# Kernel tuning notes

Hardware: AMD Instinct MI355X
Metric: run time of the kernel (lower is better)

Reference implementation:

```python
import jax, jax.numpy as jnp
import numpy as np

H = 128  # hidden_dim
COORD_CLAMP = 100.0


def _glorot(key, shape):
    fan_in, fan_out = shape[0], shape[1]
    lim = float(np.sqrt(6.0 / (fan_in + fan_out)))
    return jax.random.uniform(key, shape, jnp.float32, -lim, lim)


def setup_inputs() -> dict:
    key = jax.random.key(0)
    ks = jax.random.split(key, 20)
    B, N = 2, 512
    inp = {
        "h": jax.random.normal(ks[0], (B, N, H), jnp.float32),
        "pos": jax.random.normal(ks[1], (B, N, 3), jnp.float32),
        "vel": jax.random.normal(ks[2], (B, N, 3), jnp.float32),
        # edge_mlp: Linear(2H+2 -> H), SiLU, Linear(H -> H), SiLU
        "We1": _glorot(ks[3], (2 * H + 2, H)), "be1": jnp.zeros((H,), jnp.float32),
        "We2": _glorot(ks[4], (H, H)), "be2": jnp.zeros((H,), jnp.float32),
        # attention_mlp: Linear(H -> 1), Sigmoid
        "Wa": _glorot(ks[5], (H, 1)), "ba": jnp.zeros((1,), jnp.float32),
        # pos_mlp: Linear(H -> H), SiLU, Linear(H -> 1, no bias)
        "Wp1": _glorot(ks[6], (H, H)), "bp1": jnp.zeros((H,), jnp.float32),
        "Wp2": _glorot(ks[7], (H, 1)),
        # vel_mlp: Linear(H -> H), SiLU, Linear(H -> 1, no bias)
        "Wv1": _glorot(ks[8], (H, H)), "bv1": jnp.zeros((H,), jnp.float32),
        "Wv2": _glorot(ks[9], (H, 1)),
        # node_mlp: Linear(2H -> H), SiLU, Linear(H -> H)
        "Wn1": _glorot(ks[10], (2 * H, H)), "bn1": jnp.zeros((H,), jnp.float32),
        "Wn2": _glorot(ks[11], (H, H)), "bn2": jnp.zeros((H,), jnp.float32),
    }
    return inp


def reference(h, pos, vel, We1, be1, We2, be2, Wa, ba,
              Wp1, bp1, Wp2, Wv1, bv1, Wv2, Wn1, bn1, Wn2, bn2):
    B, N, _ = pos.shape
    # pairwise diffs: [B, N, N, 3]
    pos_diff = pos[:, :, None, :] - pos[:, None, :, :]
    vel_diff = vel[:, :, None, :] - vel[:, None, :, :]
    pos_dist_sq = jnp.sum(pos_diff ** 2, axis=-1, keepdims=True)  # [B,N,N,1]
    vel_dist_sq = jnp.sum(vel_diff ** 2, axis=-1, keepdims=True)
    h_i = jnp.broadcast_to(h[:, :, None, :], (B, N, N, H))
    h_j = jnp.broadcast_to(h[:, None, :, :], (B, N, N, H))
    edge_input = jnp.concatenate([h_i, h_j, pos_dist_sq, vel_dist_sq], axis=-1)  # [B,N,N,2H+2]
    # edge MLP
    m = jax.nn.silu(jnp.einsum('bijc,ch->bijh', edge_input, We1) + be1)
    m_ij = jax.nn.silu(jnp.einsum('bijh,hk->bijk', m, We2) + be2)
    # attention gate
    att = jax.nn.sigmoid(jnp.einsum('bijh,ho->bijo', m_ij, Wa) + ba)  # [B,N,N,1]
    m_ij = m_ij * att
    # tanh-weighted coordinate/velocity updates
    pos_w = jnp.tanh(jnp.einsum('bijh,ho->bijo', jax.nn.silu(jnp.einsum('bijh,hk->bijk', m_ij, Wp1) + bp1), Wp2))
    vel_w = jnp.tanh(jnp.einsum('bijh,ho->bijo', jax.nn.silu(jnp.einsum('bijh,hk->bijk', m_ij, Wv1) + bv1), Wv2))
    denom = jnp.float32(max(N - 1, 1))
    pos_update = jnp.sum(pos_diff * pos_w, axis=2) / denom  # [B,N,3]
    vel_update = jnp.sum(vel_diff * vel_w, axis=2) / denom
    pos_out = jnp.clip(pos + pos_update, -COORD_CLAMP, COORD_CLAMP)
    vel_out = jnp.clip(vel + vel_update, -COORD_CLAMP, COORD_CLAMP)
    # node update
    m_agg = jnp.sum(m_ij, axis=2)  # [B,N,H]
    node_input = jnp.concatenate([h, m_agg], axis=-1)  # [B,N,2H]
    h_out = jax.nn.silu(jnp.einsum('bnc,ch->bnh', node_input, Wn1) + bn1)
    h_out = jnp.einsum('bnh,hk->bnk', h_out, Wn2) + bn2
    h_out = h + h_out  # residual
    return (h_out, pos_out, vel_out)
```

## Files before the change

kernel.cpp:

```cpp
#include <hip/hip_runtime.h>
#include <hip/hip_bf16.h>

#define Hd 128
#define Nn 512
#define TJ 32
#define LSTRIDE 136

typedef __bf16 bf16x8 __attribute__((ext_vector_type(8)));
typedef float  floatx4 __attribute__((ext_vector_type(4)));

__device__ __forceinline__ float frcp(float x){ return __builtin_amdgcn_rcpf(x); }
__device__ __forceinline__ float fsilu(float x){ return x * frcp(1.f + __expf(-x)); }
__device__ __forceinline__ float fsigm(float x){ return frcp(1.f + __expf(-x)); }
__device__ __forceinline__ float ftanh(float x){ return 1.f - 2.f * frcp(__expf(2.f*x) + 1.f); }
__device__ __forceinline__ float rfl(float x){
  return __int_as_float(__builtin_amdgcn_readfirstlane(__float_as_int(x)));
}

__global__ __launch_bounds__(256) void prep(const float* __restrict__ h,
                                            const float* __restrict__ We1,
                                            const float* __restrict__ be1,
                                            const float* __restrict__ We2,
                                            const float* __restrict__ Wp1,
                                            const float* __restrict__ Wv1,
                                            float* __restrict__ A,
                                            float* __restrict__ Bm,
                                            __bf16* __restrict__ dst,
                                            float* __restrict__ zbase){
  if (blockIdx.x < 1024){
    const int row = blockIdx.x;
    const int k = threadIdx.x & 127, ch = threadIdx.x >> 7;
    __shared__ float hL[Hd];
    __shared__ float pa[2][Hd], pb[2][Hd];
    if (threadIdx.x < Hd) hL[threadIdx.x] = h[row*Hd + threadIdx.x];
    __syncthreads();
    float a0=0.f,a1=0.f, b0=0.f,b1=0.f;
    const int cbase = ch*64;
    #pragma unroll 8
    for (int cc = 0; cc < 64; cc += 2){
      const int c = cbase + cc;
      a0 += hL[c]   * We1[c*Hd + k];
      a1 += hL[c+1] * We1[(c+1)*Hd + k];
      b0 += hL[c]   * We1[(c+Hd)*Hd + k];
      b1 += hL[c+1] * We1[(c+1+Hd)*Hd + k];
    }
    pa[ch][k] = a0 + a1;
    pb[ch][k] = b0 + b1;
    __syncthreads();
    if (threadIdx.x < Hd){
      A[row*Hd + k]  = pa[0][k] + pa[1][k] + be1[k];
      Bm[row*Hd + k] = pb[0][k] + pb[1][k];
    }
  } else if (blockIdx.x < 1048){
    const int blk = blockIdx.x - 1024;
    const int which = blk >> 3, m = blk & 7;
    const float* src = (which == 0) ? We2 : (which == 1 ? Wp1 : Wv1);
    __bf16* d = dst + which * (Hd*Hd);
    #pragma unroll
    for (int it = 0; it < 8; ++it){
      const int sidx = m*2048 + it*256 + threadIdx.x;
      const int kk = sidx >> 7, cc = sidx & 127;
      const int s = kk >> 5, j = kk & 7;
      const int lane = ((kk >> 3) & 3)*16 + (cc & 15);
      const int n = cc >> 4;
      d[n*2048 + s*512 + lane*8 + j] = (__bf16)src[sidx];
    }
  } else {
    const int t0 = (blockIdx.x - 1048)*256 + threadIdx.x;
    for (int idx = t0; idx < 137216; idx += 2048) zbase[idx] = 0.f;
  }
}

__device__ __forceinline__ void gemm_kloop(const __bf16* __restrict__ buf,
                                           const bf16x8* __restrict__ Bs,
                                           int w, int lane, int q, int l15,
                                           floatx4 acc[2][2]){
  const floatx4 zero = {0.f, 0.f, 0.f, 0.f};
  #pragma unroll
  for (int m = 0; m < 2; ++m){ acc[m][0] = zero; acc[m][1] = zero; }
  #pragma unroll
  for (int s = 0; s < 4; ++s){
    bf16x8 af[2];
    #pragma unroll
    for (int m = 0; m < 2; ++m)
      af[m] = *(const bf16x8*)&buf[(16*m + l15)*LSTRIDE + s*32 + q*8];
    const bf16x8 b0 = Bs[((2*w + 0)*4 + s)*64 + lane];
    const bf16x8 b1 = Bs[((2*w + 1)*4 + s)*64 + lane];
    #pragma unroll
    for (int m = 0; m < 2; ++m){
      acc[m][0] = __builtin_amdgcn_mfma_f32_16x16x32_bf16(af[m], b0, acc[m][0], 0, 0, 0);
      acc[m][1] = __builtin_amdgcn_mfma_f32_16x16x32_bf16(af[m], b1, acc[m][1], 0, 0, 0);
    }
  }
}

__device__ __forceinline__ float fold_reduce8(float pr[8], int lane){
  #pragma unroll
  for (int k = 0; k < 4; ++k){
    const float send = (lane & 1) ? pr[k] : pr[k+4];
    const float recv = __shfl_xor(send, 1, 64);
    pr[k] = ((lane & 1) ? pr[k+4] : pr[k]) + recv;
  }
  #pragma unroll
  for (int k = 0; k < 2; ++k){
    const float send = (lane & 2) ? pr[k] : pr[k+2];
    const float recv = __shfl_xor(send, 2, 64);
    pr[k] = ((lane & 2) ? pr[k+2] : pr[k]) + recv;
  }
  {
    const float send = (lane & 4) ? pr[0] : pr[1];
    const float recv = __shfl_xor(send, 4, 64);
    pr[0] = ((lane & 4) ? pr[1] : pr[0]) + recv;
  }
  pr[0] += __shfl_xor(pr[0], 8, 64);
  return pr[0];
}
__device__ __forceinline__ int bitrev3(int x){
  return ((x&1)<<2) | (x&2) | ((x&4)>>2);
}

__device__ __forceinline__ void wdot_epilogue(floatx4 acc[2][2],
                                              const float att[2][4],
                                              const float* __restrict__ biasL,
                                              const float* __restrict__ wG,
                                              int w, int lane, int q, int l15,
                                              float (*part)[TJ]){
  float pr[8];
  #pragma unroll
  for (int k = 0; k < 8; ++k) pr[k] = 0.f;
  const int c0 = 32*w + l15, c1 = c0 + 16;
  const float bb0 = biasL[c0], bb1 = biasL[c1];
  const float ww0 = wG[c0],    ww1 = wG[c1];
  #pragma unroll
  for (int m = 0; m < 2; ++m){
    #pragma unroll
    for (int r = 0; r < 4; ++r){
      pr[4*m + r] += fsilu(fmaf(att[m][r], acc[m][0][r], bb0)) * ww0;
      pr[4*m + r] += fsilu(fmaf(att[m][r], acc[m][1][r], bb1)) * ww1;
    }
  }
  const float v = fold_reduce8(pr, lane);
  if ((lane & 15) < 8){
    const int k = bitrev3(l15 & 7);
    part[w][16*(k >> 2) + 4*q + (k & 3)] = v;
  }
}

__global__ __launch_bounds__(256) void egnn_main(
    const float* __restrict__ pos, const float* __restrict__ vel,
    const float* __restrict__ We1, const float* __restrict__ be2,
    const float* __restrict__ Wa,  const float* __restrict__ ba,
    const float* __restrict__ bp1, const float* __restrict__ Wp2,
    const float* __restrict__ bv1, const float* __restrict__ Wv2,
    const float* __restrict__ A,   const float* __restrict__ Bm,
    const __bf16* __restrict__ Wsw,
    float* __restrict__ magg, float* __restrict__ posu, float* __restrict__ velu){

  const int t    = threadIdx.x;
  const int w    = t >> 6;
  const int lane = t & 63;
  const int q    = lane >> 4;
  const int l15  = lane & 15;
  const int node = blockIdx.x >> 1;
  const int half = blockIdx.x & 1;
  const int b    = node >> 9;
  const int i    = node & (Nn - 1);

  __shared__ float AiL[Hd], wpL[Hd], wvL[Hd], be2L[Hd], bp1L[Hd], bv1L[Hd];
  __shared__ __align__(16) __bf16 bufm [TJ*LSTRIDE];
  __shared__ __align__(16) __bf16 bufij[TJ*LSTRIDE];
  __shared__ float partAtt[4][TJ], partP[4][TJ], partV[4][TJ];
  __shared__ float attL[TJ];

  if (t < Hd){
    AiL[t]  = A[node*Hd + t];
    wpL[t]  = We1[256*Hd + t];
    wvL[t]  = We1[257*Hd + t];
    be2L[t] = be2[t]; bp1L[t] = bp1[t]; bv1L[t] = bv1[t];
  }
  const float baV = ba[0];
  const float* pi = &pos[(size_t)node*3];
  const float* vi = &vel[(size_t)node*3];
  const float px = rfl(pi[0]), py = rfl(pi[1]), pz = rfl(pi[2]);
  const float ux = rfl(vi[0]), uy = rfl(vi[1]), uz = rfl(vi[2]);
  __syncthreads();

  const bf16x8* We2s = (const bf16x8*)(Wsw);
  const bf16x8* Wp1s = (const bf16x8*)(Wsw + Hd*Hd);
  const bf16x8* Wv1s = (const bf16x8*)(Wsw + 2*Hd*Hd);

  float accR[8];
  #pragma unroll
  for (int e = 0; e < 8; ++e) accR[e] = 0.f;

  for (int jt = 0; jt < (Nn/2)/TJ; ++jt){
    const int j0 = half*(Nn/2) + jt * TJ;

    {
      const int j = t >> 3, seg = t & 7;
      const int jg = j0 + j;
      const float* pj = &pos[(size_t)(b*Nn + jg)*3];
      const float* vj = &vel[(size_t)(b*Nn + jg)*3];
      const float dx = px - pj[0], dy = py - pj[1], dz = pz - pj[2];
      const float dp = dx*dx + dy*dy + dz*dz;
      const float ex = ux - vj[0], ey = uy - vj[1], ez = uz - vj[2];
      const float dv = ex*ex + ey*ey + ez*ez;
      const floatx4* A4  = (const floatx4*)&AiL[seg*16];
      const floatx4* wp4 = (const floatx4*)&wpL[seg*16];
      const floatx4* wv4 = (const floatx4*)&wvL[seg*16];
      const floatx4* Bp4 = (const floatx4*)&Bm[((size_t)(b*Nn + jg))*Hd + seg*16];
      bf16x8* dstp = (bf16x8*)&bufm[j*LSTRIDE + seg*16];
      #pragma unroll
      for (int u = 0; u < 2; ++u){
        union { bf16x8 v; __hip_bfloat162 h2[4]; } o;
        #pragma unroll
        for (int v2 = 0; v2 < 2; ++v2){
          const floatx4 av = A4[u*2+v2], wpv = wp4[u*2+v2];
          const floatx4 wvv = wv4[u*2+v2], bv = Bp4[u*2+v2];
          float x[4];
          #pragma unroll
          for (int e = 0; e < 4; ++e)
            x[e] = fsilu(av[e] + bv[e] + dp*wpv[e] + dv*wvv[e]);
          o.h2[v2*2+0] = __float22bfloat162_rn(make_float2(x[0], x[1]));
          o.h2[v2*2+1] = __float22bfloat162_rn(make_float2(x[2], x[3]));
        }
        dstp[u] = o.v;
      }
    }
    __syncthreads();

    {
      floatx4 acc[2][2];
      gemm_kloop(bufm, We2s, w, lane, q, l15, acc);
      float aw[8];
      #pragma unroll
      for (int k = 0; k < 8; ++k) aw[k] = 0.f;
      const int c0 = 32*w + l15, c1 = c0 + 16;
      const float bb0 = be2L[c0], bb1 = be2L[c1];
      const float wa0 = Wa[c0],   wa1 = Wa[c1];
      #pragma unroll
      for (int m = 0; m < 2; ++m){
        #pragma unroll
        for (int r = 0; r < 4; ++r){
          const int row = 16*m + 4*q + r;
          const float sv0 = fsilu(acc[m][0][r] + bb0);
          const float sv1 = fsilu(acc[m][1][r] + bb1);
          bufij[row*LSTRIDE + c0] = (__bf16)sv0;
          bufij[row*LSTRIDE + c1] = (__bf16)sv1;
          aw[4*m + r] += sv0*wa0 + sv1*wa1;
        }
      }
      const float v = fold_reduce8(aw, lane);
      if (l15 < 8){
        const int k = bitrev3(l15);
        partAtt[w][16*(k >> 2) + 4*q + (k & 3)] = v;
      }
    }
    __syncthreads();

    {
      const int rowX = (16*(l15 & 3) + 4*q + (l15 >> 2)) & (TJ - 1);
      const float attv = fsigm(partAtt[0][rowX] + partAtt[1][rowX] +
                               partAtt[2][rowX] + partAtt[3][rowX] + baV);
      if (w == 3 && (l15 & 3) < 2) attL[rowX] = attv;
      floatx4 acc[2][2];
      gemm_kloop(bufij, Wp1s, w, lane, q, l15, acc);
      float att[2][4];
      #pragma unroll
      for (int m = 0; m < 2; ++m)
        #pragma unroll
        for (int r = 0; r < 4; ++r)
          att[m][r] = __shfl(attv, 16*q + 4*r + m, 64);
      wdot_epilogue(acc, att, bp1L, Wp2, w, lane, q, l15, partP);
      gemm_kloop(bufij, Wv1s, w, lane, q, l15, acc);
      wdot_epilogue(acc, att, bv1L, Wv2, w, lane, q, l15, partV);
    }
    __syncthreads();

    if (w == 0){
      if (lane < TJ){
        const int jg = j0 + lane;
        const float* pj = &pos[(size_t)(b*Nn + jg)*3];
        const float s4 = partP[0][lane] + partP[1][lane] + partP[2][lane] + partP[3][lane];
        const float pw = ftanh(s4);
        accR[0] += (px - pj[0]) * pw;
        accR[1] += (py - pj[1]) * pw;
        accR[2] += (pz - pj[2]) * pw;
      }
    } else if (w == 1){
      if (lane < TJ){
        const int jg = j0 + lane;
        const float* vj = &vel[(size_t)(b*Nn + jg)*3];
        const float s4 = partV[0][lane] + partV[1][lane] + partV[2][lane] + partV[3][lane];
        const float vw = ftanh(s4);
        accR[0] += (ux - vj[0]) * vw;
        accR[1] += (uy - vj[1]) * vw;
        accR[2] += (uz - vj[2]) * vw;
      }
    } else {
      const int sg   = (w - 2)*8 + (lane & 7);
      const int jsub = lane >> 3;
      #pragma unroll
      for (int jj = 0; jj < 4; ++jj){
        const int j = jj*8 + jsub;
        const float aj = attL[j];
        const bf16x8 v = *(const bf16x8*)&bufij[j*LSTRIDE + sg*8];
        #pragma unroll
        for (int e = 0; e < 8; ++e) accR[e] += aj * (float)v[e];
      }
    }
  }

  if (w == 0 || w == 1){
    float v0 = accR[0], v1 = accR[1], v2 = accR[2];
    #pragma unroll
    for (int off = 1; off < 64; off <<= 1){
      v0 += __shfl_xor(v0, off, 64);
      v1 += __shfl_xor(v1, off, 64);
      v2 += __shfl_xor(v2, off, 64);
    }
    if (lane == 0){
      float* dst = (w == 0) ? &posu[node*3] : &velu[node*3];
      atomicAdd(&dst[0], v0);
      atomicAdd(&dst[1], v1);
      atomicAdd(&dst[2], v2);
    }
  } else {
    const int sg = (w - 2)*8 + (lane & 7);
    #pragma unroll
    for (int off = 8; off < 64; off <<= 1){
      #pragma unroll
      for (int e = 0; e < 8; ++e) accR[e] += __shfl_xor(accR[e], off, 64);
    }
    if ((lane >> 3) == 0){
      #pragma unroll
      for (int e = 0; e < 8; ++e)
        atomicAdd(&magg[node*Hd + sg*8 + e], accR[e]);
    }
  }
}

__global__ __launch_bounds__(256) void egnn_final(
    const float* __restrict__ h, const float* __restrict__ pos, const float* __restrict__ vel,
    const float* __restrict__ Wn1, const float* __restrict__ bn1,
    const float* __restrict__ Wn2, const float* __restrict__ bn2,
    const float* __restrict__ magg, const float* __restrict__ posu,
    const float* __restrict__ velu, float* __restrict__ out){
  const int row = blockIdx.x;
  const int t = threadIdx.x;
  const int k = t & 127, ch = t >> 7;
  __shared__ float ni[2*Hd];
  __shared__ float p1[2][Hd], t1[Hd];
  ni[t] = (t < Hd) ? h[row*Hd + t] : magg[row*Hd + (t - Hd)];
  __syncthreads();
  {
    float a0=0.f,a1=0.f,a2=0.f,a3=0.f;
    const int cb = ch*Hd;
    #pragma unroll 8
    for (int cc = 0; cc < Hd; cc += 4){
      a0 += ni[cb+cc+0] * Wn1[(cb+cc+0)*Hd + k];
      a1 += ni[cb+cc+1] * Wn1[(cb+cc+1)*Hd + k];
      a2 += ni[cb+cc+2] * Wn1[(cb+cc+2)*Hd + k];
      a3 += ni[cb+cc+3] * Wn1[(cb+cc+3)*Hd + k];
    }
    p1[ch][k] = (a0+a1)+(a2+a3);
  }
  __syncthreads();
  if (t < Hd) t1[t] = fsilu(p1[0][t] + p1[1][t] + bn1[t]);
  __syncthreads();
  {
    float a0=0.f,a1=0.f,a2=0.f,a3=0.f;
    const int cb = ch*64;
    #pragma unroll 8
    for (int cc = 0; cc < 64; cc += 4){
      a0 += t1[cb+cc+0] * Wn2[(cb+cc+0)*Hd + k];
      a1 += t1[cb+cc+1] * Wn2[(cb+cc+1)*Hd + k];
      a2 += t1[cb+cc+2] * Wn2[(cb+cc+2)*Hd + k];
      a3 += t1[cb+cc+3] * Wn2[(cb+cc+3)*Hd + k];
    }
    p1[ch][k] = (a0+a1)+(a2+a3);
  }
  __syncthreads();
  if (t < Hd){
    out[row*Hd + t] = ni[t] + p1[0][t] + p1[1][t] + bn2[t];
  } else if (t < Hd + 3){
    const int d = t - Hd;
    const float v = pos[row*3 + d] + posu[row*3 + d] * (1.f/511.f);
    out[2*Nn*Hd + row*3 + d] = fminf(fmaxf(v, -100.f), 100.f);
  } else if (t < Hd + 6){
    const int d = t - Hd - 3;
    const float v = vel[row*3 + d] + velu[row*3 + d] * (1.f/511.f);
    out[2*Nn*Hd + 2*Nn*3 + row*3 + d] = fminf(fmaxf(v, -100.f), 100.f);
  }
}

extern "C" void kernel_launch(void* const* d_in, const int* in_sizes, int n_in,
                              void* d_out, int out_size, void* d_ws, size_t ws_size,
                              hipStream_t stream){
  const float* h   = (const float*)d_in[0];
  const float* pos = (const float*)d_in[1];
  const float* vel = (const float*)d_in[2];
  const float* We1 = (const float*)d_in[3];
  const float* be1 = (const float*)d_in[4];
  const float* We2 = (const float*)d_in[5];
  const float* be2 = (const float*)d_in[6];
  const float* Wa  = (const float*)d_in[7];
  const float* ba  = (const float*)d_in[8];
  const float* Wp1 = (const float*)d_in[9];
  const float* bp1 = (const float*)d_in[10];
  const float* Wp2 = (const float*)d_in[11];
  const float* Wv1 = (const float*)d_in[12];
  const float* bv1 = (const float*)d_in[13];
  const float* Wv2 = (const float*)d_in[14];
  const float* Wn1 = (const float*)d_in[15];
  const float* bn1 = (const float*)d_in[16];
  const float* Wn2 = (const float*)d_in[17];
  const float* bn2 = (const float*)d_in[18];

  float* ws = (float*)d_ws;
  float*  A    = ws;
  float*  Bmm  = ws + 131072;
  float*  magg = ws + 262144;
  float*  posu = ws + 393216;
  float*  velu = ws + 396288;
  __bf16* Wsw  = (__bf16*)(ws + 399360);

  prep      <<<dim3(1056), dim3(256), 0, stream>>>(h, We1, be1, We2, Wp1, Wv1,
                                                   A, Bmm, Wsw, magg);
  egnn_main <<<dim3(2048), dim3(256), 0, stream>>>(pos, vel, We1, be2, Wa, ba, bp1, Wp2,
                                                   bv1, Wv2, A, Bmm, Wsw, magg, posu, velu);
  egnn_final<<<dim3(1024), dim3(256), 0, stream>>>(h, pos, vel, Wn1, bn1, Wn2, bn2,
                                                   magg, posu, velu, (float*)d_out);
}
```

Before: 248.3 us.

## Fuse node MLP into main kernel via last-block counter and batch prep rows

Drops the separate egnn_final launch. The last of the two half-blocks per node, found with an atomic counter and a threadfence, now runs the node MLP and the position/velocity clamp inside egnn_main. The prep kernel now handles 4 rows per block so each We1 load is reused across rows, which cuts the grid from 1056 to 288 blocks. This saves a kernel launch and a global round trip, at the cost of extra atomics and fences in every main block. The zeroing range is extended so the counters are cleared each call.

```diff
diff --git a/kernel.cpp b/kernel.cpp
--- a/kernel.cpp
+++ b/kernel.cpp
@@ -27,32 +27,40 @@
                                             float* __restrict__ Bm,
                                             __bf16* __restrict__ dst,
                                             float* __restrict__ zbase){
-  if (blockIdx.x < 1024){
-    const int row = blockIdx.x;
+  if (blockIdx.x < 256){
+    const int r0 = blockIdx.x * 4;
     const int k = threadIdx.x & 127, ch = threadIdx.x >> 7;
-    __shared__ float hL[Hd];
-    __shared__ float pa[2][Hd], pb[2][Hd];
-    if (threadIdx.x < Hd) hL[threadIdx.x] = h[row*Hd + threadIdx.x];
+    __shared__ float hL[4][Hd];
+    __shared__ float pa[2][4][Hd], pb[2][4][Hd];
+    for (int idx = threadIdx.x; idx < 4*Hd; idx += 256)
+      hL[idx >> 7][idx & 127] = h[r0*Hd + idx];
     __syncthreads();
-    float a0=0.f,a1=0.f, b0=0.f,b1=0.f;
+    float a[4] = {0.f,0.f,0.f,0.f}, bb[4] = {0.f,0.f,0.f,0.f};
     const int cbase = ch*64;
-    #pragma unroll 8
-    for (int cc = 0; cc < 64; cc += 2){
+    #pragma unroll 4
+    for (int cc = 0; cc < 64; ++cc){
       const int c = cbase + cc;
-      a0 += hL[c]   * We1[c*Hd + k];
-      a1 += hL[c+1] * We1[(c+1)*Hd + k];
-      b0 += hL[c]   * We1[(c+Hd)*Hd + k];
-      b1 += hL[c+1] * We1[(c+1+Hd)*Hd + k];
-    }
-    pa[ch][k] = a0 + a1;
-    pb[ch][k] = b0 + b1;
+      const float wa = We1[c*Hd + k];
+      const float wb = We1[(c + Hd)*Hd + k];
+      #pragma unroll
+      for (int rr = 0; rr < 4; ++rr){
+        a[rr]  += hL[rr][c] * wa;
+        bb[rr] += hL[rr][c] * wb;
+      }
+    }
+    #pragma unroll
+    for (int rr = 0; rr < 4; ++rr){ pa[ch][rr][k] = a[rr]; pb[ch][rr][k] = bb[rr]; }
     __syncthreads();
     if (threadIdx.x < Hd){
-      A[row*Hd + k]  = pa[0][k] + pa[1][k] + be1[k];
-      Bm[row*Hd + k] = pb[0][k] + pb[1][k];
-    }
-  } else if (blockIdx.x < 1048){
-    const int blk = blockIdx.x - 1024;
+      const float be = be1[k];
+      #pragma unroll
+      for (int rr = 0; rr < 4; ++rr){
+        A[(r0+rr)*Hd + k]  = pa[0][rr][k] + pa[1][rr][k] + be;
+        Bm[(r0+rr)*Hd + k] = pb[0][rr][k] + pb[1][rr][k];
+      }
+    }
+  } else if (blockIdx.x < 280){
+    const int blk = blockIdx.x - 256;
     const int which = blk >> 3, m = blk & 7;
     const float* src = (which == 0) ? We2 : (which == 1 ? Wp1 : Wv1);
     __bf16* d = dst + which * (Hd*Hd);
@@ -66,8 +74,8 @@
       d[n*2048 + s*512 + lane*8 + j] = (__bf16)src[sidx];
     }
   } else {
-    const int t0 = (blockIdx.x - 1048)*256 + threadIdx.x;
-    for (int idx = t0; idx < 137216; idx += 2048) zbase[idx] = 0.f;
+    const int t0 = (blockIdx.x - 280)*256 + threadIdx.x;
+    for (int idx = t0; idx < 138240; idx += 2048) zbase[idx] = 0.f;
   }
 }
 
@@ -147,14 +155,18 @@
 }
 
 __global__ __launch_bounds__(256) void egnn_main(
+    const float* __restrict__ h,
     const float* __restrict__ pos, const float* __restrict__ vel,
     const float* __restrict__ We1, const float* __restrict__ be2,
     const float* __restrict__ Wa,  const float* __restrict__ ba,
     const float* __restrict__ bp1, const float* __restrict__ Wp2,
     const float* __restrict__ bv1, const float* __restrict__ Wv2,
+    const float* __restrict__ Wn1, const float* __restrict__ bn1,
+    const float* __restrict__ Wn2, const float* __restrict__ bn2,
     const float* __restrict__ A,   const float* __restrict__ Bm,
     const __bf16* __restrict__ Wsw,
-    float* __restrict__ magg, float* __restrict__ posu, float* __restrict__ velu){
+    float* __restrict__ magg, float* __restrict__ posu, float* __restrict__ velu,
+    int* __restrict__ cnt, float* __restrict__ out){
 
   const int t    = threadIdx.x;
   const int w    = t >> 6;
@@ -164,13 +176,13 @@
   const int node = blockIdx.x >> 1;
   const int half = blockIdx.x & 1;
   const int b    = node >> 9;
-  const int i    = node & (Nn - 1);
 
   __shared__ float AiL[Hd], wpL[Hd], wvL[Hd], be2L[Hd], bp1L[Hd], bv1L[Hd];
   __shared__ __align__(16) __bf16 bufm [TJ*LSTRIDE];
   __shared__ __align__(16) __bf16 bufij[TJ*LSTRIDE];
   __shared__ float partAtt[4][TJ], partP[4][TJ], partV[4][TJ];
   __shared__ float attL[TJ];
+  __shared__ int lastS;
 
   if (t < Hd){
     AiL[t]  = A[node*Hd + t];
@@ -338,59 +350,67 @@
         atomicAdd(&magg[node*Hd + sg*8 + e], accR[e]);
     }
   }
-}
-
-__global__ __launch_bounds__(256) void egnn_final(
-    const float* __restrict__ h, const float* __restrict__ pos, const float* __restrict__ vel,
-    const float* __restrict__ Wn1, const float* __restrict__ bn1,
-    const float* __restrict__ Wn2, const float* __restrict__ bn2,
-    const float* __restrict__ magg, const float* __restrict__ posu,
-    const float* __restrict__ velu, float* __restrict__ out){
-  const int row = blockIdx.x;
-  const int t = threadIdx.x;
-  const int k = t & 127, ch = t >> 7;
-  __shared__ float ni[2*Hd];
-  __shared__ float p1[2][Hd], t1[Hd];
-  ni[t] = (t < Hd) ? h[row*Hd + t] : magg[row*Hd + (t - Hd)];
+
+  __threadfence();
+  __syncthreads();
+  if (t == 0)
+    lastS = __hip_atomic_fetch_add(&cnt[node], 1, __ATOMIC_ACQ_REL,
+                                   __HIP_MEMORY_SCOPE_AGENT);
+  __syncthreads();
+  if (lastS == 0) return;
+
+  float* sF = (float*)bufm;
+  if (t < Hd){
+    sF[t] = h[(size_t)node*Hd + t];
+  } else {
+    sF[t] = __hip_atomic_load(&magg[(size_t)node*Hd + (t - Hd)],
+                              __ATOMIC_RELAXED, __HIP_MEMORY_SCOPE_AGENT);
+  }
   __syncthreads();
   {
+    const int k = t & 127, ch = t >> 7;
+    const int cb = ch*Hd;
     float a0=0.f,a1=0.f,a2=0.f,a3=0.f;
-    const int cb = ch*Hd;
     #pragma unroll 8
     for (int cc = 0; cc < Hd; cc += 4){
-      a0 += ni[cb+cc+0] * Wn1[(cb+cc+0)*Hd + k];
-      a1 += ni[cb+cc+1] * Wn1[(cb+cc+1)*Hd + k];
-      a2 += ni[cb+cc+2] * Wn1[(cb+cc+2)*Hd + k];
-      a3 += ni[cb+cc+3] * Wn1[(cb+cc+3)*Hd + k];
-    }
-    p1[ch][k] = (a0+a1)+(a2+a3);
-  }
-  __syncthreads();
-  if (t < Hd) t1[t] = fsilu(p1[0][t] + p1[1][t] + bn1[t]);
+      a0 += sF[cb+cc+0] * Wn1[(cb+cc+0)*Hd + k];
+      a1 += sF[cb+cc+1] * Wn1[(cb+cc+1)*Hd + k];
+      a2 += sF[cb+cc+2] * Wn1[(cb+cc+2)*Hd + k];
+      a3 += sF[cb+cc+3] * Wn1[(cb+cc+3)*Hd + k];
+    }
+    sF[256 + ch*128 + k] = (a0+a1)+(a2+a3);
+  }
+  __syncthreads();
+  if (t < Hd) sF[512 + t] = fsilu(sF[256 + t] + sF[384 + t] + bn1[t]);
   __syncthreads();
   {
+    const int k = t & 127, ch = t >> 7;
+    const int cb = ch*64;
     float a0=0.f,a1=0.f,a2=0.f,a3=0.f;
-    const int cb = ch*64;
     #pragma unroll 8
     for (int cc = 0; cc < 64; cc += 4){
-      a0 += t1[cb+cc+0] * Wn2[(cb+cc+0)*Hd + k];
-      a1 += t1[cb+cc+1] * Wn2[(cb+cc+1)*Hd + k];
-      a2 += t1[cb+cc+2] * Wn2[(cb+cc+2)*Hd + k];
-      a3 += t1[cb+cc+3] * Wn2[(cb+cc+3)*Hd + k];
-    }
-    p1[ch][k] = (a0+a1)+(a2+a3);
+      a0 += sF[512+cb+cc+0] * Wn2[(cb+cc+0)*Hd + k];
+      a1 += sF[512+cb+cc+1] * Wn2[(cb+cc+1)*Hd + k];
+      a2 += sF[512+cb+cc+2] * Wn2[(cb+cc+2)*Hd + k];
+      a3 += sF[512+cb+cc+3] * Wn2[(cb+cc+3)*Hd + k];
+    }
+    sF[256 + ch*128 + k] = (a0+a1)+(a2+a3);
   }
   __syncthreads();
   if (t < Hd){
-    out[row*Hd + t] = ni[t] + p1[0][t] + p1[1][t] + bn2[t];
+    out[(size_t)node*Hd + t] = sF[t] + sF[256 + t] + sF[384 + t] + bn2[t];
   } else if (t < Hd + 3){
     const int d = t - Hd;
-    const float v = pos[row*3 + d] + posu[row*3 + d] * (1.f/511.f);
-    out[2*Nn*Hd + row*3 + d] = fminf(fmaxf(v, -100.f), 100.f);
+    const float pu = __hip_atomic_load(&posu[node*3 + d], __ATOMIC_RELAXED,
+                                       __HIP_MEMORY_SCOPE_AGENT);
+    const float v = pos[node*3 + d] + pu * (1.f/511.f);
+    out[2*Nn*Hd + node*3 + d] = fminf(fmaxf(v, -100.f), 100.f);
   } else if (t < Hd + 6){
     const int d = t - Hd - 3;
-    const float v = vel[row*3 + d] + velu[row*3 + d] * (1.f/511.f);
-    out[2*Nn*Hd + 2*Nn*3 + row*3 + d] = fminf(fmaxf(v, -100.f), 100.f);
+    const float vu = __hip_atomic_load(&velu[node*3 + d], __ATOMIC_RELAXED,
+                                       __HIP_MEMORY_SCOPE_AGENT);
+    const float v = vel[node*3 + d] + vu * (1.f/511.f);
+    out[2*Nn*Hd + 2*Nn*3 + node*3 + d] = fminf(fmaxf(v, -100.f), 100.f);
   }
 }
 
@@ -423,12 +443,13 @@
   float*  magg = ws + 262144;
   float*  posu = ws + 393216;
   float*  velu = ws + 396288;
-  __bf16* Wsw  = (__bf16*)(ws + 399360);
-
-  prep      <<<dim3(1056), dim3(256), 0, stream>>>(h, We1, be1, We2, Wp1, Wv1,
-                                                   A, Bmm, Wsw, magg);
-  egnn_main <<<dim3(2048), dim3(256), 0, stream>>>(pos, vel, We1, be2, Wa, ba, bp1, Wp2,
-                                                   bv1, Wv2, A, Bmm, Wsw, magg, posu, velu);
-  egnn_final<<<dim3(1024), dim3(256), 0, stream>>>(h, pos, vel, Wn1, bn1, Wn2, bn2,
-                                                   magg, posu, velu, (float*)d_out);
-}
+  int*    cnt  = (int*)(ws + 399360);
+  __bf16* Wsw  = (__bf16*)(ws + 400384);
+
+  prep     <<<dim3(288),  dim3(256), 0, stream>>>(h, We1, be1, We2, Wp1, Wv1,
+                                                  A, Bmm, Wsw, magg);
+  egnn_main<<<dim3(2048), dim3(256), 0, stream>>>(h, pos, vel, We1, be2, Wa, ba, bp1, Wp2,
+                                                  bv1, Wv2, Wn1, bn1, Wn2, bn2,
+                                                  A, Bmm, Wsw, magg, posu, velu,
+                                                  cnt, (float*)d_out);
+}
```

Measured after the change: 360.2 us. +45.1%, slower.
